# Optimization experiments

Hardware: AMD Instinct MI355X
Metric: run time of the kernel (lower is better)

Reference implementation:

```python
import jax, jax.numpy as jnp
import numpy as np

B, T = 16384, 64
VOCAB, D, HD, FF = 10, 3, 4, 2
EPS = 1e-6


def _rms(x, w):
    return x * jax.lax.rsqrt(jnp.mean(x * x, axis=-1, keepdims=True) + EPS) * w


def _rope(x, theta=3.0):
    # x: [..., T, HD]; interleaved rotary, matching the torch RotaryEmbedding
    t = jnp.arange(x.shape[-2], dtype=x.dtype)
    inv_freq = 1.0 / theta ** (jnp.arange(0, HD, 2, dtype=x.dtype) / HD)  # [HD/2]
    freqs = jnp.outer(t, inv_freq)                                        # [T, HD/2]
    cos_f, sin_f = jnp.cos(freqs), jnp.sin(freqs)
    x1, x2 = x[..., ::2], x[..., 1::2]
    rot = jnp.stack([x1 * cos_f - x2 * sin_f, x1 * sin_f + x2 * cos_f], axis=-1)
    return rot.reshape(x.shape)


def setup_inputs() -> dict:
    key = jax.random.key(0)
    ks = jax.random.split(key, 12)
    f32 = jnp.float32
    return {
        "idx": jax.random.randint(ks[0], (B, T), 0, VOCAB, dtype=jnp.int32),
        "arc_A": jnp.asarray(2.5, f32),
        "arc_start": jnp.asarray(-1.2, f32),
        "arc_stride": jnp.asarray(0.29, f32),
        "w_ln1": jnp.ones((D,), f32) + 0.1 * jax.random.normal(ks[1], (D,), f32),
        "w_ln2": jnp.ones((D,), f32) + 0.1 * jax.random.normal(ks[2], (D,), f32),
        "w_lnf": jnp.ones((D,), f32) + 0.1 * jax.random.normal(ks[3], (D,), f32),
        "w_qn": jnp.ones((HD,), f32) + 0.1 * jax.random.normal(ks[4], (HD,), f32),
        "Wq": jax.random.normal(ks[5], (HD, D), f32) * 0.5,
        "Wk": jax.random.normal(ks[6], (HD, D), f32) * 0.5,
        "Wg": jax.random.normal(ks[7], (FF, D), f32) * 0.5,
        "Wu": jax.random.normal(ks[8], (FF, D), f32) * 0.5,
        "Wd": jax.random.normal(ks[9], (D, FF), f32) * 0.5,
    }


def reference(idx, arc_A, arc_start, arc_stride, w_ln1, w_ln2, w_lnf, w_qn,
              Wq, Wk, Wg, Wu, Wd):
    dt = arc_A.dtype
    # circular-arc token embedding table [VOCAB, 2]
    digits = jnp.arange(VOCAB, dtype=dt)
    angles = arc_start + digits * arc_stride
    table = jnp.stack([arc_A * jnp.cos(angles), arc_A * jnp.sin(angles)], axis=1)

    tok = table[idx]                                              # [B,T,2]
    pe = jnp.sin(jnp.arange(T, dtype=dt) * jnp.exp(jnp.asarray(-np.log(10000.0), dt)))
    pos = jnp.broadcast_to(pe[None, :, None], (idx.shape[0], T, 1))
    x = jnp.concatenate([tok, pos], axis=-1)                      # [B,T,3]

    h = _rms(x, w_ln1)
    q = _rms(h @ Wq.T, w_qn)                                      # [B,T,HD]
    k = _rms(h @ Wk.T, w_qn)
    v = h @ Wk.T                                                  # v = k pre-norm? no: v = k.clone() BEFORE q_norm
    q = _rope(q)
    k = _rope(k)

    scale = HD ** (-0.5)
    scores = jnp.einsum("btd,bsd->bts", q, k) * scale             # [B,T,T]
    causal = jnp.triu(jnp.ones((T, T), dtype=bool), k=1)
    scores = jnp.where(causal, -jnp.inf, scores)
    attn = jax.nn.softmax(scores, axis=-1)
    out = jnp.einsum("bts,bsd->btd", attn, v)                     # [B,T,HD]

    x = x + out @ Wq                                              # F.linear(out, Wq.T) == out @ Wq
    h = _rms(x, w_ln2)
    x = x + (jax.nn.silu(h @ Wg.T) * (h @ Wu.T)) @ Wd.T
    x = _rms(x, w_lnf)
    return x[..., :2] @ table.T                                   # [B,T,VOCAB]
```

## Files before the change

### kernel.cpp

```cpp
#include <hip/hip_runtime.h>
#include <math.h>


namespace {
constexpr int kVocab = 10;
constexpr float kEps = 1e-6f;
constexpr int kWaves = 4;

typedef __attribute__((ext_vector_type(8)))  short short8;
typedef __attribute__((ext_vector_type(16))) float float16;

constexpr int kOffQh  = 0;
constexpr int kOffQl  = 512;
constexpr int kOffKh  = 1024;
constexpr int kOffKl  = 1536;
constexpr int kOffO   = 0;
constexpr int kOffP   = 2048;
constexpr int kOffVt  = 11264;
constexpr int kWaveLds = 12544;
constexpr int kPP = 72;
constexpr int kOP = 76;

__device__ __forceinline__ unsigned bf16_rn(float x) {
    const unsigned u = __float_as_uint(x);
    return (u + 0x7fffu + ((u >> 16) & 1u)) >> 16;
}
__device__ __forceinline__ unsigned pk_bf16(float a, float b) {
    return bf16_rn(a) | (bf16_rn(b) << 16);
}
__device__ __forceinline__ float bf_lo(unsigned u) { return __uint_as_float(u << 16); }
__device__ __forceinline__ float bf_hi(unsigned u) { return __uint_as_float(u & 0xffff0000u); }

__device__ __forceinline__ float16 mfma(short8 a, short8 b, float16 c) {
    return __builtin_amdgcn_mfma_f32_32x32x16_bf16(a, b, c, 0, 0, 0);
}

__device__ __forceinline__ short8 tok_frag(const char* wbase, int off, int tok, bool lo_half) {
    uint2 r = *(const uint2*)(wbase + off + tok * 8);
    uint4 t;
    t.x = lo_half ? r.x : 0u;
    t.y = lo_half ? r.y : 0u;
    t.z = 0u; t.w = 0u;
    return __builtin_bit_cast(short8, t);
}

template<int TM, int TN, bool MASKED>
__device__ __forceinline__ void exp_store(const float16& S, ushort* P, int tloc, int h, int m) {
    const int t = TN * 32 + tloc;
#pragma unroll
    for (int c = 0; c < 4; ++c) {
        float e[4];
#pragma unroll
        for (int j = 0; j < 4; ++j) {
            float sc = S[4 * c + j];
            if (MASKED) sc = ((j + 8 * c) <= m) ? sc : -INFINITY;
            e[j] = __builtin_amdgcn_exp2f(sc);
        }
        uint2 w;
        w.x = pk_bf16(e[0], e[1]);
        w.y = pk_bf16(e[2], e[3]);
        *(uint2*)(P + t * kPP + TM * 32 + 8 * c + 4 * h) = w;
    }
}

__global__ __launch_bounds__(256, 3) void adder_model_kernel(
    const int* __restrict__ idx,
    const float* __restrict__ p_arcA,
    const float* __restrict__ p_arcStart,
    const float* __restrict__ p_arcStride,
    const float* __restrict__ w_ln1,
    const float* __restrict__ w_ln2,
    const float* __restrict__ w_lnf,
    const float* __restrict__ w_qn,
    const float* __restrict__ Wq,
    const float* __restrict__ Wk,
    const float* __restrict__ Wg,
    const float* __restrict__ Wu,
    const float* __restrict__ Wd,
    float* __restrict__ out)
{
    __shared__ __align__(16) char smem[kWaves][kWaveLds];
    __shared__ float table_s[kVocab * 2];

    const int lane = threadIdx.x & 63;
    const int wid  = threadIdx.x >> 6;
    char* wbase = &smem[wid][0];

    if (threadIdx.x < kVocab) {
        const float ang = p_arcStart[0] + (float)threadIdx.x * p_arcStride[0];
        const float A = p_arcA[0];
        table_s[2 * threadIdx.x]     = A * __cosf(ang);
        table_s[2 * threadIdx.x + 1] = A * __sinf(ang);
    }
    __syncthreads();

    float tb[2 * kVocab];
#pragma unroll
    for (int d = 0; d < 2 * kVocab; ++d) tb[d] = table_s[d];

    const float t_f = (float)lane;
    const float pe  = __sinf(t_f * 1e-4f);
    const float c0  = __cosf(t_f);
    const float s0  = __sinf(t_f);
    const float ang1 = t_f * 0.57735026918962576f;
    const float c1  = __cosf(ang1);
    const float s1  = __sinf(ang1);

    const float wl1_0 = w_ln1[0], wl1_1 = w_ln1[1], wl1_2 = w_ln1[2];
    const float wl2_0 = w_ln2[0], wl2_1 = w_ln2[1], wl2_2 = w_ln2[2];
    const float wlf0 = w_lnf[0], wlf1 = w_lnf[1];
    const float wqn0 = w_qn[0], wqn1 = w_qn[1], wqn2 = w_qn[2], wqn3 = w_qn[3];
    const float Wq00 = Wq[0],  Wq01 = Wq[1],  Wq02 = Wq[2];
    const float Wq10 = Wq[3],  Wq11 = Wq[4],  Wq12 = Wq[5];
    const float Wq20 = Wq[6],  Wq21 = Wq[7],  Wq22 = Wq[8];
    const float Wq30 = Wq[9],  Wq31 = Wq[10], Wq32 = Wq[11];
    const float Wk00 = Wk[0],  Wk01 = Wk[1],  Wk02 = Wk[2];
    const float Wk10 = Wk[3],  Wk11 = Wk[4],  Wk12 = Wk[5];
    const float Wk20 = Wk[6],  Wk21 = Wk[7],  Wk22 = Wk[8];
    const float Wk30 = Wk[9],  Wk31 = Wk[10], Wk32 = Wk[11];
    const float Wg00 = Wg[0],  Wg01 = Wg[1],  Wg02 = Wg[2];
    const float Wg10 = Wg[3],  Wg11 = Wg[4],  Wg12 = Wg[5];
    const float Wu00 = Wu[0],  Wu01 = Wu[1],  Wu02 = Wu[2];
    const float Wu10 = Wu[3],  Wu11 = Wu[4],  Wu12 = Wu[5];
    const float Wd00 = Wd[0],  Wd01 = Wd[1];
    const float Wd10 = Wd[2],  Wd11 = Wd[3];
    const float Wd20 = Wd[4],  Wd21 = Wd[5];

    const int row = (int)blockIdx.x * kWaves + wid;

    const int tix = idx[(size_t)row * 64 + lane];
    const float x0i = table_s[2 * tix];
    const float x1i = table_s[2 * tix + 1];
    const float x2i = pe;

    const float r1 = __builtin_amdgcn_rsqf((x0i*x0i + x1i*x1i + x2i*x2i) * (1.0f/3.0f) + kEps);
    const float h0 = x0i * r1 * wl1_0;
    const float h1 = x1i * r1 * wl1_1;
    const float h2 = x2i * r1 * wl1_2;

    const float qp0 = h0*Wq00 + h1*Wq01 + h2*Wq02;
    const float qp1 = h0*Wq10 + h1*Wq11 + h2*Wq12;
    const float qp2 = h0*Wq20 + h1*Wq21 + h2*Wq22;
    const float qp3 = h0*Wq30 + h1*Wq31 + h2*Wq32;
    const float v0 = h0*Wk00 + h1*Wk01 + h2*Wk02;
    const float v1 = h0*Wk10 + h1*Wk11 + h2*Wk12;
    const float v2 = h0*Wk20 + h1*Wk21 + h2*Wk22;
    const float v3 = h0*Wk30 + h1*Wk31 + h2*Wk32;

    const float rq = __builtin_amdgcn_rsqf((qp0*qp0 + qp1*qp1 + qp2*qp2 + qp3*qp3) * 0.25f + kEps);
    const float rk = __builtin_amdgcn_rsqf((v0*v0 + v1*v1 + v2*v2 + v3*v3) * 0.25f + kEps);
    const float qn0 = qp0*rq*wqn0, qn1 = qp1*rq*wqn1, qn2 = qp2*rq*wqn2, qn3 = qp3*rq*wqn3;
    const float kn0 = v0*rk*wqn0,  kn1 = v1*rk*wqn1,  kn2 = v2*rk*wqn2,  kn3 = v3*rk*wqn3;

    constexpr float kQS = 0.72134752044448170f;
    const float q0 = (qn0*c0 - qn1*s0) * kQS;
    const float q1 = (qn0*s0 + qn1*c0) * kQS;
    const float q2 = (qn2*c1 - qn3*s1) * kQS;
    const float q3 = (qn2*s1 + qn3*c1) * kQS;
    const float k0 = kn0*c0 - kn1*s0;
    const float k1 = kn0*s0 + kn1*c0;
    const float k2 = kn2*c1 - kn3*s1;
    const float k3 = kn2*s1 + kn3*c1;

    uint2 qh, ql, kh, kl;
    qh.x = pk_bf16(q0, q1); qh.y = pk_bf16(q2, q3);
    ql.x = pk_bf16(q0 - bf_lo(qh.x), q1 - bf_hi(qh.x));
    ql.y = pk_bf16(q2 - bf_lo(qh.y), q3 - bf_hi(qh.y));
    kh.x = pk_bf16(k0, k1); kh.y = pk_bf16(k2, k3);
    kl.x = pk_bf16(k0 - bf_lo(kh.x), k1 - bf_hi(kh.x));
    kl.y = pk_bf16(k2 - bf_lo(kh.y), k3 - bf_hi(kh.y));
    *(uint2*)(wbase + kOffQh + lane * 8) = qh;
    *(uint2*)(wbase + kOffQl + lane * 8) = ql;
    *(uint2*)(wbase + kOffKh + lane * 8) = kh;
    *(uint2*)(wbase + kOffKl + lane * 8) = kl;

    ushort* Vt = (ushort*)(wbase + kOffVt);
    Vt[0 * kPP + lane] = (ushort)bf16_rn(v0);
    Vt[1 * kPP + lane] = (ushort)bf16_rn(v1);
    Vt[2 * kPP + lane] = (ushort)bf16_rn(v2);
    Vt[3 * kPP + lane] = (ushort)bf16_rn(v3);
    Vt[4 * kPP + lane] = 0x3F80;
    __threadfence_block();

    const int tloc = lane & 31;
    const bool loh = lane < 32;
    const int h    = lane >> 5;
    const int m    = tloc - 4 * h;

    const short8 aKh0 = tok_frag(wbase, kOffKh, tloc,      loh);
    const short8 aKl0 = tok_frag(wbase, kOffKl, tloc,      loh);
    const short8 aKh1 = tok_frag(wbase, kOffKh, tloc + 32, loh);
    const short8 aKl1 = tok_frag(wbase, kOffKl, tloc + 32, loh);
    const short8 bQh0 = tok_frag(wbase, kOffQh, tloc,      loh);
    const short8 bQl0 = tok_frag(wbase, kOffQl, tloc,      loh);
    const short8 bQh1 = tok_frag(wbase, kOffQh, tloc + 32, loh);
    const short8 bQl1 = tok_frag(wbase, kOffQl, tloc + 32, loh);

    float16 Z = {0,0,0,0,0,0,0,0,0,0,0,0,0,0,0,0};
    float16 S00 = mfma(aKl0, bQh0, mfma(aKh0, bQl0, mfma(aKh0, bQh0, Z)));
    float16 S01 = mfma(aKl0, bQh1, mfma(aKh0, bQl1, mfma(aKh0, bQh1, Z)));
    float16 S11 = mfma(aKl1, bQh1, mfma(aKh1, bQl1, mfma(aKh1, bQh1, Z)));

    ushort* P = (ushort*)(wbase + kOffP);
    exp_store<0, 0, true >(S00, P, tloc, h, m);
    exp_store<0, 1, false>(S01, P, tloc, h, m);
    exp_store<1, 1, true >(S11, P, tloc, h, m);
    __threadfence_block();

    short8 vb[4];
#pragma unroll
    for (int kc = 0; kc < 4; ++kc)
        vb[kc] = __builtin_bit_cast(short8,
            *(const uint4*)(Vt + (tloc & 7) * kPP + 16 * kc + 8 * h));

    float16 acc0 = Z, acc1 = Z;
#pragma unroll
    for (int kc = 0; kc < 2; ++kc) {
        short8 pa = __builtin_bit_cast(short8,
            *(const uint4*)(P + tloc * kPP + 16 * kc + 8 * h));
        acc0 = mfma(pa, vb[kc], acc0);
    }
#pragma unroll
    for (int kc = 0; kc < 4; ++kc) {
        short8 pa = __builtin_bit_cast(short8,
            *(const uint4*)(P + (tloc + 32) * kPP + 16 * kc + 8 * h));
        acc1 = mfma(pa, vb[kc], acc1);
    }

    float* Ol = (float*)(wbase + kOffO);
    if (tloc < 5) {
#pragma unroll
        for (int c = 0; c < 4; ++c) {
            float4 w0 = make_float4(acc0[4*c], acc0[4*c+1], acc0[4*c+2], acc0[4*c+3]);
            *(float4*)(Ol + tloc * kOP +      8 * c + 4 * h) = w0;
            float4 w1 = make_float4(acc1[4*c], acc1[4*c+1], acc1[4*c+2], acc1[4*c+3]);
            *(float4*)(Ol + tloc * kOP + 32 + 8 * c + 4 * h) = w1;
        }
    }
    __threadfence_block();

    const float o0r = Ol[0 * kOP + lane];
    const float o1r = Ol[1 * kOP + lane];
    const float o2r = Ol[2 * kOP + lane];
    const float o3r = Ol[3 * kOP + lane];
    const float lr  = Ol[4 * kOP + lane];

    const float invl = __builtin_amdgcn_rcpf(lr);
    const float o0 = o0r * invl, o1 = o1r * invl, o2 = o2r * invl, o3 = o3r * invl;

    const float xa0 = x0i + o0*Wq00 + o1*Wq10 + o2*Wq20 + o3*Wq30;
    const float xa1 = x1i + o0*Wq01 + o1*Wq11 + o2*Wq21 + o3*Wq31;
    const float xa2 = x2i + o0*Wq02 + o1*Wq12 + o2*Wq22 + o3*Wq32;

    const float r2 = __builtin_amdgcn_rsqf((xa0*xa0 + xa1*xa1 + xa2*xa2) * (1.0f/3.0f) + kEps);
    const float hh0 = xa0*r2*wl2_0, hh1 = xa1*r2*wl2_1, hh2 = xa2*r2*wl2_2;
    const float g0 = hh0*Wg00 + hh1*Wg01 + hh2*Wg02;
    const float g1 = hh0*Wg10 + hh1*Wg11 + hh2*Wg12;
    const float u0 = hh0*Wu00 + hh1*Wu01 + hh2*Wu02;
    const float u1 = hh0*Wu10 + hh1*Wu11 + hh2*Wu12;
    constexpr float kL2E = 1.4426950408889634f;
    const float f0 = g0 * __builtin_amdgcn_rcpf(1.0f + __builtin_amdgcn_exp2f(-g0 * kL2E)) * u0;
    const float f1 = g1 * __builtin_amdgcn_rcpf(1.0f + __builtin_amdgcn_exp2f(-g1 * kL2E)) * u1;
    const float xf0 = xa0 + f0*Wd00 + f1*Wd01;
    const float xf1 = xa1 + f0*Wd10 + f1*Wd11;
    const float xf2 = xa2 + f0*Wd20 + f1*Wd21;

    const float rf = __builtin_amdgcn_rsqf((xf0*xf0 + xf1*xf1 + xf2*xf2) * (1.0f/3.0f) + kEps);
    const float y0 = xf0 * rf * wlf0;
    const float y1 = xf1 * rf * wlf1;

    float2* op = (float2*)(out + (size_t)(row * 64 + lane) * kVocab);
#pragma unroll
    for (int d = 0; d < kVocab / 2; ++d) {
        float2 o2v;
        o2v.x = y0 * tb[4*d]     + y1 * tb[4*d + 1];
        o2v.y = y0 * tb[4*d + 2] + y1 * tb[4*d + 3];
        op[d] = o2v;
    }
}
}

extern "C" void kernel_launch(void* const* d_in, const int* in_sizes, int n_in,
                              void* d_out, int out_size, void* d_ws, size_t ws_size,
                              hipStream_t stream) {
    (void)in_sizes; (void)n_in; (void)d_ws; (void)ws_size; (void)out_size;
    const int*   idx       = (const int*)  d_in[0];
    const float* arcA      = (const float*)d_in[1];
    const float* arcStart  = (const float*)d_in[2];
    const float* arcStride = (const float*)d_in[3];
    const float* w_ln1     = (const float*)d_in[4];
    const float* w_ln2     = (const float*)d_in[5];
    const float* w_lnf     = (const float*)d_in[6];
    const float* w_qn      = (const float*)d_in[7];
    const float* Wq        = (const float*)d_in[8];
    const float* Wk        = (const float*)d_in[9];
    const float* Wg        = (const float*)d_in[10];
    const float* Wu        = (const float*)d_in[11];
    const float* Wd        = (const float*)d_in[12];
    float* out = (float*)d_out;

    dim3 grid(4096), block(256);
    hipLaunchKernelGGL(adder_model_kernel, grid, block, 0, stream,
                       idx, arcA, arcStart, arcStride,
                       w_ln1, w_ln2, w_lnf, w_qn, Wq, Wk, Wg, Wu, Wd, out);
}
```

Before: 112.8 us.

## Shrink per-wave LDS with split P buffers, raise occupancy, cheapen bf16 rounding

Splits the probability buffer into a narrow buffer for the first query block and a wide one for the second, reusing the Q/K fragment space. This cuts per-wave LDS from 12544 to 8320 bytes, and launch bounds go from 3 to 4 blocks per CU. It also replaces round-to-nearest-even bf16 conversion with a cheaper round-half-up, loads the embedding and output table with vector LDS reads instead of keeping the table in registers, and adds a fence before the P writes overwrite the fragment area. The tradeoffs are slightly different rounding and the correctness risk of aliasing P0 onto the Q/K storage.

```diff
diff --git a/kernel.cpp b/kernel.cpp
--- a/kernel.cpp
+++ b/kernel.cpp
@@ -14,19 +14,23 @@
 constexpr int kOffQl  = 512;
 constexpr int kOffKh  = 1024;
 constexpr int kOffKl  = 1536;
+constexpr int kOffP0  = 0;
+constexpr int kOffP1  = 2560;
+constexpr int kOffVt  = 7168;
 constexpr int kOffO   = 0;
-constexpr int kOffP   = 2048;
-constexpr int kOffVt  = 11264;
-constexpr int kWaveLds = 12544;
-constexpr int kPP = 72;
-constexpr int kOP = 76;
-
-__device__ __forceinline__ unsigned bf16_rn(float x) {
-    const unsigned u = __float_as_uint(x);
-    return (u + 0x7fffu + ((u >> 16) & 1u)) >> 16;
+constexpr int kWaveLds = 8320;
+constexpr int kP0P = 40;
+constexpr int kP1P = 72;
+constexpr int kVtP = 72;
+constexpr int kOP  = 76;
+
+__device__ __forceinline__ unsigned bf16_1(float a) {
+    return (__float_as_uint(a) + 0x8000u) >> 16;
 }
 __device__ __forceinline__ unsigned pk_bf16(float a, float b) {
-    return bf16_rn(a) | (bf16_rn(b) << 16);
+    const unsigned au = __float_as_uint(a) + 0x8000u;
+    const unsigned bu = __float_as_uint(b) + 0x8000u;
+    return (au >> 16) | (bu & 0xffff0000u);
 }
 __device__ __forceinline__ float bf_lo(unsigned u) { return __uint_as_float(u << 16); }
 __device__ __forceinline__ float bf_hi(unsigned u) { return __uint_as_float(u & 0xffff0000u); }
@@ -44,9 +48,8 @@
     return __builtin_bit_cast(short8, t);
 }
 
-template<int TM, int TN, bool MASKED>
-__device__ __forceinline__ void exp_store(const float16& S, ushort* P, int tloc, int h, int m) {
-    const int t = TN * 32 + tloc;
+template<bool MASKED>
+__device__ __forceinline__ void exp_store(const float16& S, ushort* rowbase, int h, int m) {
 #pragma unroll
     for (int c = 0; c < 4; ++c) {
         float e[4];
@@ -59,11 +62,11 @@
         uint2 w;
         w.x = pk_bf16(e[0], e[1]);
         w.y = pk_bf16(e[2], e[3]);
-        *(uint2*)(P + t * kPP + TM * 32 + 8 * c + 4 * h) = w;
-    }
-}
-
-__global__ __launch_bounds__(256, 3) void adder_model_kernel(
+        *(uint2*)(rowbase + 8 * c + 4 * h) = w;
+    }
+}
+
+__global__ __launch_bounds__(256, 4) void adder_model_kernel(
     const int* __restrict__ idx,
     const float* __restrict__ p_arcA,
     const float* __restrict__ p_arcStart,
@@ -80,7 +83,7 @@
     float* __restrict__ out)
 {
     __shared__ __align__(16) char smem[kWaves][kWaveLds];
-    __shared__ float table_s[kVocab * 2];
+    __shared__ __align__(16) float table_s[kVocab * 2];
 
     const int lane = threadIdx.x & 63;
     const int wid  = threadIdx.x >> 6;
@@ -93,10 +96,6 @@
         table_s[2 * threadIdx.x + 1] = A * __sinf(ang);
     }
     __syncthreads();
-
-    float tb[2 * kVocab];
-#pragma unroll
-    for (int d = 0; d < 2 * kVocab; ++d) tb[d] = table_s[d];
 
     const float t_f = (float)lane;
     const float pe  = __sinf(t_f * 1e-4f);
@@ -129,9 +128,8 @@
     const int row = (int)blockIdx.x * kWaves + wid;
 
     const int tix = idx[(size_t)row * 64 + lane];
-    const float x0i = table_s[2 * tix];
-    const float x1i = table_s[2 * tix + 1];
-    const float x2i = pe;
+    const float2 emb = *(const float2*)(table_s + 2 * tix);
+    const float x0i = emb.x, x1i = emb.y, x2i = pe;
 
     const float r1 = __builtin_amdgcn_rsqf((x0i*x0i + x1i*x1i + x2i*x2i) * (1.0f/3.0f) + kEps);
     const float h0 = x0i * r1 * wl1_0;
@@ -175,17 +173,17 @@
     *(uint2*)(wbase + kOffKl + lane * 8) = kl;
 
     ushort* Vt = (ushort*)(wbase + kOffVt);
-    Vt[0 * kPP + lane] = (ushort)bf16_rn(v0);
-    Vt[1 * kPP + lane] = (ushort)bf16_rn(v1);
-    Vt[2 * kPP + lane] = (ushort)bf16_rn(v2);
-    Vt[3 * kPP + lane] = (ushort)bf16_rn(v3);
-    Vt[4 * kPP + lane] = 0x3F80;
+    Vt[0 * kVtP + lane] = (ushort)bf16_1(v0);
+    Vt[1 * kVtP + lane] = (ushort)bf16_1(v1);
+    Vt[2 * kVtP + lane] = (ushort)bf16_1(v2);
+    Vt[3 * kVtP + lane] = (ushort)bf16_1(v3);
+    Vt[4 * kVtP + lane] = (ushort)0x3F80;
     __threadfence_block();
 
-    const int tloc = lane & 31;
-    const bool loh = lane < 32;
-    const int h    = lane >> 5;
-    const int m    = tloc - 4 * h;
+    const int  tloc = lane & 31;
+    const bool loh  = lane < 32;
+    const int  h    = lane >> 5;
+    const int  m    = tloc - 4 * h;
 
     const short8 aKh0 = tok_frag(wbase, kOffKh, tloc,      loh);
     const short8 aKl0 = tok_frag(wbase, kOffKl, tloc,      loh);
@@ -195,35 +193,37 @@
     const short8 bQl0 = tok_frag(wbase, kOffQl, tloc,      loh);
     const short8 bQh1 = tok_frag(wbase, kOffQh, tloc + 32, loh);
     const short8 bQl1 = tok_frag(wbase, kOffQl, tloc + 32, loh);
+    __threadfence_block();
 
     float16 Z = {0,0,0,0,0,0,0,0,0,0,0,0,0,0,0,0};
     float16 S00 = mfma(aKl0, bQh0, mfma(aKh0, bQl0, mfma(aKh0, bQh0, Z)));
     float16 S01 = mfma(aKl0, bQh1, mfma(aKh0, bQl1, mfma(aKh0, bQh1, Z)));
     float16 S11 = mfma(aKl1, bQh1, mfma(aKh1, bQl1, mfma(aKh1, bQh1, Z)));
 
-    ushort* P = (ushort*)(wbase + kOffP);
-    exp_store<0, 0, true >(S00, P, tloc, h, m);
-    exp_store<0, 1, false>(S01, P, tloc, h, m);
-    exp_store<1, 1, true >(S11, P, tloc, h, m);
+    ushort* P0 = (ushort*)(wbase + kOffP0);
+    ushort* P1 = (ushort*)(wbase + kOffP1);
+    exp_store<true >(S00, P0 + tloc * kP0P,      h, m);
+    exp_store<false>(S01, P1 + tloc * kP1P,      h, m);
+    exp_store<true >(S11, P1 + tloc * kP1P + 32, h, m);
     __threadfence_block();
 
     short8 vb[4];
 #pragma unroll
     for (int kc = 0; kc < 4; ++kc)
         vb[kc] = __builtin_bit_cast(short8,
-            *(const uint4*)(Vt + (tloc & 7) * kPP + 16 * kc + 8 * h));
+            *(const uint4*)(Vt + (tloc & 7) * kVtP + 16 * kc + 8 * h));
 
     float16 acc0 = Z, acc1 = Z;
 #pragma unroll
     for (int kc = 0; kc < 2; ++kc) {
         short8 pa = __builtin_bit_cast(short8,
-            *(const uint4*)(P + tloc * kPP + 16 * kc + 8 * h));
+            *(const uint4*)(P0 + tloc * kP0P + 16 * kc + 8 * h));
         acc0 = mfma(pa, vb[kc], acc0);
     }
 #pragma unroll
     for (int kc = 0; kc < 4; ++kc) {
         short8 pa = __builtin_bit_cast(short8,
-            *(const uint4*)(P + (tloc + 32) * kPP + 16 * kc + 8 * h));
+            *(const uint4*)(P1 + tloc * kP1P + 16 * kc + 8 * h));
         acc1 = mfma(pa, vb[kc], acc1);
     }
 
@@ -269,14 +269,15 @@
     const float y0 = xf0 * rf * wlf0;
     const float y1 = xf1 * rf * wlf1;
 
+    const float4* tb4 = (const float4*)table_s;
+    const float4 T0 = tb4[0], T1 = tb4[1], T2 = tb4[2], T3 = tb4[3], T4 = tb4[4];
+
     float2* op = (float2*)(out + (size_t)(row * 64 + lane) * kVocab);
-#pragma unroll
-    for (int d = 0; d < kVocab / 2; ++d) {
-        float2 o2v;
-        o2v.x = y0 * tb[4*d]     + y1 * tb[4*d + 1];
-        o2v.y = y0 * tb[4*d + 2] + y1 * tb[4*d + 3];
-        op[d] = o2v;
-    }
+    op[0] = float2{y0*T0.x + y1*T0.y, y0*T0.z + y1*T0.w};
+    op[1] = float2{y0*T1.x + y1*T1.y, y0*T1.z + y1*T1.w};
+    op[2] = float2{y0*T2.x + y1*T2.y, y0*T2.z + y1*T2.w};
+    op[3] = float2{y0*T3.x + y1*T3.y, y0*T3.z + y1*T3.w};
+    op[4] = float2{y0*T4.x + y1*T4.y, y0*T4.z + y1*T4.w};
 }
 }
 
```

Measured after the change: 109.4 us. 3.1% less time.
